# Performance work log

Hardware: AMD Instinct MI355X
Metric: run time of the kernel (lower is better)

## Reference

```python
import jax, jax.numpy as jnp
import numpy as np

T = 4096
MOL = 2048
DESC = 6
NSOL = 5
H = 2048
D_BLOCK = MOL + DESC            # 2054
FUSE = D_BLOCK * (1 + NSOL)     # 12324
D_IN = FUSE + 1                 # 12325
BOUNDARY_RF = 0.5
CLAMP_LO, CLAMP_HI = 1e-4, 1.0 - 1e-4


def setup_inputs() -> dict:
    key = jax.random.key(0)
    ks = jax.random.split(key, 32)
    s = 0.02  # weight init scale for numerical stability
    d = {
        "mol_vec": jax.random.normal(ks[0], (MOL,), jnp.float32),
        "solvent_seq": jax.random.uniform(ks[1], (T, NSOL), jnp.float32),
        "desc_seq": jax.random.normal(ks[2], (T, DESC), jnp.float32),
        "rf_true": jax.random.uniform(ks[3], (T,), jnp.float32),
        "solvent_vecs": jax.random.normal(ks[4], (NSOL, MOL), jnp.float32),
    }
    wshapes = [
        ("Wf0", (H, D_IN)), ("Wf1", (H, H)), ("Wf2", (H, H)), ("Wof", (1, H)),
        ("Wb0", (H, D_IN)), ("Wb1", (H, H)), ("Wb2", (H, H)), ("Wob", (1, H)),
    ]
    for i, (name, shp) in enumerate(wshapes):
        d[name] = jax.random.normal(ks[5 + i], shp, jnp.float32) * s
    for name, shp in [("bf0", (H,)), ("bf1", (H,)), ("bf2", (H,)), ("bof", (1,)),
                      ("bb0", (H,)), ("bb1", (H,)), ("bb2", (H,)), ("bob", (1,))]:
        d[name] = jnp.zeros(shp, jnp.float32)
    return d


def _step_features(mol_vec, solvent_seq, desc_seq, solvent_vecs):
    # mol_vec [MOL]; solvent_seq [T,NSOL]; desc_seq [T,DESC]; solvent_vecs [NSOL,MOL]
    mol_cat = jnp.concatenate(
        [jnp.broadcast_to(mol_vec, (T, MOL)), desc_seq], axis=-1)  # [T, D_BLOCK]
    scaled = solvent_seq[:, :, None] * solvent_vecs[None, :, :]      # [T,NSOL,MOL]
    sol_block = jnp.concatenate(
        [scaled, jnp.broadcast_to(desc_seq[:, None, :], (T, NSOL, DESC))], axis=-1)
    sol_flat = sol_block.reshape(T, NSOL * D_BLOCK)
    return jnp.concatenate([mol_cat, sol_flat], axis=-1)             # [T, FUSE]


def _trunk(x, W0, b0, W1, b1, W2, b2):
    # 3 Linear+GELU blocks (dropout is identity in eval)
    h = jax.nn.gelu(x @ W0.T + b0, approximate=False)
    h = jax.nn.gelu(h @ W1.T + b1, approximate=False)
    h = jax.nn.gelu(h @ W2.T + b2, approximate=False)
    return h


def reference(mol_vec, solvent_seq, desc_seq, rf_true, solvent_vecs,
              Wf0, bf0, Wf1, bf1, Wf2, bf2, Wof, bof,
              Wb0, bb0, Wb1, bb1, Wb2, bb2, Wob, bob):
    x = _step_features(mol_vec, solvent_seq, desc_seq, solvent_vecs)  # [T, FUSE]
    rf = jax.lax.stop_gradient(rf_true)  # teacher signal is detached
    b = jnp.asarray([BOUNDARY_RF], dtype=x.dtype)
    prev = jnp.concatenate([b, rf[:-1]])  # fwd branch sees rf_true[t-1]
    nxt = jnp.concatenate([rf[1:], b])    # bwd branch sees rf_true[t+1]

    inp_f = jnp.concatenate([x, prev[:, None]], axis=-1)  # [T, D_IN]
    inp_b = jnp.concatenate([x, nxt[:, None]], axis=-1)

    hf = _trunk(inp_f, Wf0, bf0, Wf1, bf1, Wf2, bf2)
    hb = _trunk(inp_b, Wb0, bb0, Wb1, bb1, Wb2, bb2)
    rf_fwd = (hf @ Wof.T + bof).squeeze(-1)  # [T]
    rf_bwd = (hb @ Wob.T + bob).squeeze(-1)
    rf_fwd = jnp.clip(rf_fwd, CLAMP_LO, CLAMP_HI)
    rf_bwd = jnp.clip(rf_bwd, CLAMP_LO, CLAMP_HI)
    return rf_fwd, rf_bwd
```

## Files before the change

kernel.cpp:

```cpp
#include <hip/hip_runtime.h>
#include <hip/hip_fp16.h>
#include <math.h>

#define T_DIM 4096
#define MOL_N 2048
#define DESC_N 6
#define NSOL_N 5
#define H_DIM 2048
#define DBLK 2054
#define D_IN_N 12325
#define GK 2048

typedef _Float16 f16x8 __attribute__((ext_vector_type(8)));
typedef float f32x4 __attribute__((ext_vector_type(4)));

__device__ __forceinline__ float gelu_f(float x) {
    float v = x * (1.5957691f + 0.0713548f * x * x);
    float e = __expf(-v);
    return x / (1.0f + e);
}

__global__ __launch_bounds__(256) void fold3_kernel(
    const float* __restrict__ W0f, const float* __restrict__ W0b,
    const float* __restrict__ b0f, const float* __restrict__ b0b,
    const float* __restrict__ mol, const float* __restrict__ sv,
    float* __restrict__ fold_f, float* __restrict__ fold_b)
{
    __shared__ float red[4];
    const int r = blockIdx.x;
    const int s = blockIdx.y;
    const int z = r >> 11, h = r & 2047;
    const int tid = threadIdx.x;
    const float* __restrict__ W0 = z ? W0b : W0f;
    const float* __restrict__ b0 = z ? b0b : b0f;
    float* __restrict__ fold = z ? fold_b : fold_f;
    const float* __restrict__ row = W0 + (size_t)h * D_IN_N + (size_t)s * DBLK;
    const float* __restrict__ xp = (s == 0) ? mol : (sv + (size_t)(s - 1) * MOL_N);

    float acc = 0.f;
    #pragma unroll
    for (int k = 0; k < 8; ++k) {
        const int c = tid + k * 256;
        acc += row[c] * xp[c];
    }
    #pragma unroll
    for (int off = 32; off >= 1; off >>= 1)
        acc += __shfl_xor(acc, off, 64);
    const int lane = tid & 63, wave = tid >> 6;
    if (lane == 0) red[wave] = acc;
    __syncthreads();
    if (tid == 0) {
        float v = red[0] + red[1] + red[2] + red[3];
        if (s == 0) fold[h] = v + b0[h];
        else fold[(size_t)s * H_DIM + h] = v;
    }
    if (s == 0 && tid >= 64 && tid < 70) {
        const int j = tid - 64;
        const float* __restrict__ rw = W0 + (size_t)h * D_IN_N;
        float w = rw[MOL_N + j];
        #pragma unroll
        for (int ss = 1; ss <= 5; ++ss) w += rw[(size_t)DBLK * ss + MOL_N + j];
        fold[(size_t)(6 + j) * H_DIM + h] = w;
    }
    if (s == 0 && tid == 70) {
        const float* __restrict__ rw = W0 + (size_t)h * D_IN_N;
        fold[(size_t)12 * H_DIM + h] = rw[D_IN_N - 1];
    }
}

__global__ __launch_bounds__(256) void conv_kernel(
    const float* __restrict__ W1f, const float* __restrict__ W2f,
    const float* __restrict__ W1b, const float* __restrict__ W2b,
    _Float16* __restrict__ Wc)
{
    const int b = blockIdx.x;
    const int z = b >> 10;
    const float* __restrict__ src = (z == 0) ? W1f : (z == 1) ? W2f : (z == 2) ? W1b : W2b;
    _Float16* __restrict__ dst = Wc + (size_t)z * H_DIM * H_DIM;
    const int base4 = (b & 1023) * 1024;
    struct h4 { _Float16 a, b, c, d; };
    #pragma unroll
    for (int k = 0; k < 4; ++k) {
        const int i4 = base4 + k * 256 + threadIdx.x;
        float4 v = ((const float4*)src)[i4];
        h4 o;
        o.a = (_Float16)v.x; o.b = (_Float16)v.y; o.c = (_Float16)v.z; o.d = (_Float16)v.w;
        ((h4*)dst)[i4] = o;
    }
}

__global__ __launch_bounds__(256) void h0_kernel(
    const float* __restrict__ fold_f, const float* __restrict__ fold_b,
    const float* __restrict__ desc, const float* __restrict__ sol,
    const float* __restrict__ rf,
    _Float16* __restrict__ h0f, _Float16* __restrict__ h0b)
{
    const int z = blockIdx.z;
    const float* __restrict__ fold = z ? fold_b : fold_f;
    _Float16* __restrict__ h0 = z ? h0b : h0f;
    const int hb = blockIdx.x * 1024 + threadIdx.x * 4;
    const int tbase = blockIdx.y * 64;

    float c0a[4], wpa[4], ua[NSOL_N][4], wda[DESC_N][4];
    {
        float4 v = *(const float4*)&fold[hb];
        c0a[0] = v.x; c0a[1] = v.y; c0a[2] = v.z; c0a[3] = v.w;
        v = *(const float4*)&fold[(size_t)12 * H_DIM + hb];
        wpa[0] = v.x; wpa[1] = v.y; wpa[2] = v.z; wpa[3] = v.w;
        #pragma unroll
        for (int s = 0; s < NSOL_N; ++s) {
            v = *(const float4*)&fold[(size_t)(1 + s) * H_DIM + hb];
            ua[s][0] = v.x; ua[s][1] = v.y; ua[s][2] = v.z; ua[s][3] = v.w;
        }
        #pragma unroll
        for (int j = 0; j < DESC_N; ++j) {
            v = *(const float4*)&fold[(size_t)(6 + j) * H_DIM + hb];
            wda[j][0] = v.x; wda[j][1] = v.y; wda[j][2] = v.z; wda[j][3] = v.w;
        }
    }

    struct h4s { _Float16 a, b, c, d; };
    for (int i = 0; i < 64; ++i) {
        const int t = tbase + i;
        float pv;
        if (z == 0) pv = (t == 0) ? 0.5f : rf[t - 1];
        else        pv = (t == T_DIM - 1) ? 0.5f : rf[t + 1];
        float sl[NSOL_N], dc[DESC_N];
        #pragma unroll
        for (int s = 0; s < NSOL_N; ++s) sl[s] = sol[t * NSOL_N + s];
        #pragma unroll
        for (int j = 0; j < DESC_N; ++j) dc[j] = desc[t * DESC_N + j];
        float o[4];
        #pragma unroll
        for (int e = 0; e < 4; ++e) {
            float pre = c0a[e] + wpa[e] * pv;
            #pragma unroll
            for (int s = 0; s < NSOL_N; ++s) pre += ua[s][e] * sl[s];
            #pragma unroll
            for (int j = 0; j < DESC_N; ++j) pre += wda[j][e] * dc[j];
            o[e] = gelu_f(pre);
        }
        h4s ov;
        ov.a = (_Float16)o[0]; ov.b = (_Float16)o[1];
        ov.c = (_Float16)o[2]; ov.d = (_Float16)o[3];
        *(h4s*)&h0[(size_t)t * H_DIM + hb] = ov;
    }
}

__device__ __forceinline__ void gemm_core256(
    const _Float16* __restrict__ A, const _Float16* __restrict__ W,
    const int m0, const int n0, char* sc, f32x4 (&acc)[8][4])
{
    const int tid = threadIdx.x;
    const int wave = tid >> 6;
    const int lane = tid & 63;
    const int t15 = lane & 15;
    const int quad = lane >> 4;
    const int wr = wave >> 2;
    const int wc = wave & 3;
    const int poff = (quad ^ ((t15 >> 1) & 3)) * 16;
    const int aoff0 = (wr * 128 + t15) * 64 + poff;
    const int boff0 = 16384 + (wc * 64 + t15) * 64 + poff;

    const _Float16* gsrc[4];
    #pragma unroll
    for (int ld = 0; ld < 4; ++ld) {
        const int j = (ld & 1) * 512 + tid;
        const int r = j >> 2;
        const int c = (j & 3) ^ ((r >> 1) & 3);
        gsrc[ld] = ((ld < 2) ? (A + (size_t)(m0 + r) * GK)
                             : (W + (size_t)(n0 + r) * GK)) + c * 8;
    }

    #pragma unroll
    for (int mi = 0; mi < 8; ++mi)
        #pragma unroll
        for (int ni = 0; ni < 4; ++ni)
            acc[mi][ni] = (f32x4){0.f, 0.f, 0.f, 0.f};

#define STAGE_T(kt, b) do { \
    char* _db = sc + (b) * 32768; \
    const int _ko = (kt) * 32; \
    __builtin_amdgcn_global_load_lds((const __attribute__((address_space(1))) void*)(gsrc[0] + _ko), (__attribute__((address_space(3))) void*)(_db + wave * 1024), 16, 0, 0); \
    __builtin_amdgcn_global_load_lds((const __attribute__((address_space(1))) void*)(gsrc[1] + _ko), (__attribute__((address_space(3))) void*)(_db + 8192 + wave * 1024), 16, 0, 0); \
    __builtin_amdgcn_global_load_lds((const __attribute__((address_space(1))) void*)(gsrc[2] + _ko), (__attribute__((address_space(3))) void*)(_db + 16384 + wave * 1024), 16, 0, 0); \
    __builtin_amdgcn_global_load_lds((const __attribute__((address_space(1))) void*)(gsrc[3] + _ko), (__attribute__((address_space(3))) void*)(_db + 24576 + wave * 1024), 16, 0, 0); \
} while (0)

#define COMPUTE_T(b) do { \
    const char* _db = sc + (b) * 32768; \
    f16x8 aF[8], bF[4]; \
    _Pragma("unroll") \
    for (int mi = 0; mi < 8; ++mi) aF[mi] = *(const f16x8*)(_db + aoff0 + mi * 1024); \
    _Pragma("unroll") \
    for (int ni = 0; ni < 4; ++ni) bF[ni] = *(const f16x8*)(_db + boff0 + ni * 1024); \
    __builtin_amdgcn_s_setprio(1); \
    _Pragma("unroll") \
    for (int mi = 0; mi < 8; ++mi) { \
        _Pragma("unroll") \
        for (int ni = 0; ni < 4; ++ni) \
            acc[mi][ni] = __builtin_amdgcn_mfma_f32_16x16x32_f16(aF[mi], bF[ni], acc[mi][ni], 0, 0, 0); \
    } \
    __builtin_amdgcn_s_setprio(0); \
    asm volatile("s_waitcnt lgkmcnt(0)" ::: "memory"); \
} while (0)

    STAGE_T(0, 0); STAGE_T(1, 1); STAGE_T(2, 2);

    #pragma unroll 1
    for (int k4 = 0; k4 < 60; k4 += 4) {
        asm volatile("s_waitcnt vmcnt(8)" ::: "memory");
        __builtin_amdgcn_s_barrier();
        STAGE_T(k4 + 3, 3); COMPUTE_T(0);
        asm volatile("s_waitcnt vmcnt(8)" ::: "memory");
        __builtin_amdgcn_s_barrier();
        STAGE_T(k4 + 4, 0); COMPUTE_T(1);
        asm volatile("s_waitcnt vmcnt(8)" ::: "memory");
        __builtin_amdgcn_s_barrier();
        STAGE_T(k4 + 5, 1); COMPUTE_T(2);
        asm volatile("s_waitcnt vmcnt(8)" ::: "memory");
        __builtin_amdgcn_s_barrier();
        STAGE_T(k4 + 6, 2); COMPUTE_T(3);
    }
    asm volatile("s_waitcnt vmcnt(8)" ::: "memory");
    __builtin_amdgcn_s_barrier();
    STAGE_T(63, 3); COMPUTE_T(0);
    asm volatile("s_waitcnt vmcnt(8)" ::: "memory");
    __builtin_amdgcn_s_barrier();
    COMPUTE_T(1);
    asm volatile("s_waitcnt vmcnt(4)" ::: "memory");
    __builtin_amdgcn_s_barrier();
    COMPUTE_T(2);
    asm volatile("s_waitcnt vmcnt(0)" ::: "memory");
    __builtin_amdgcn_s_barrier();
    COMPUTE_T(3);

#undef STAGE_T
#undef COMPUTE_T
}

__device__ __forceinline__ void tile_map(int bid, int& z, int& m0, int& n0, int& n_tile)
{
    const int xcd = bid & 7;
    const int slot = bid >> 3;
    z = xcd & 1;
    const int q = xcd >> 1;
    m0 = (slot & 15) * 256;
    n_tile = q * 2 + (slot >> 4);
    n0 = n_tile * 256;
}

__global__ __launch_bounds__(512, 2) void gemm1_kernel(
    const _Float16* __restrict__ Af, const _Float16* __restrict__ Ab,
    const _Float16* __restrict__ Wfp, const _Float16* __restrict__ Wbp,
    const float* __restrict__ bfp, const float* __restrict__ bbp,
    _Float16* __restrict__ Cf, _Float16* __restrict__ Cb)
{
    __shared__ _Float16 smem[65536];
    char* sc = (char*)smem;
    int z, m0, n0, n_tile;
    tile_map(blockIdx.x, z, m0, n0, n_tile);

    const _Float16* __restrict__ A = z ? Ab : Af;
    const _Float16* __restrict__ W = z ? Wbp : Wfp;
    const float* __restrict__ bias = z ? bbp : bfp;
    _Float16* __restrict__ C = z ? Cb : Cf;

    f32x4 acc[8][4];
    gemm_core256(A, W, m0, n0, sc, acc);

    const int tid = threadIdx.x;
    const int wave = tid >> 6, lane = tid & 63;
    const int colC = lane & 15, quad = lane >> 4;
    const int wr = wave >> 2, wc = wave & 3;
    #pragma unroll
    for (int ni = 0; ni < 4; ++ni) {
        const int n = n0 + wc * 64 + ni * 16 + colC;
        const float bv = bias[n];
        #pragma unroll
        for (int mi = 0; mi < 8; ++mi) {
            const int mb = m0 + wr * 128 + mi * 16 + quad * 4;
            #pragma unroll
            for (int r = 0; r < 4; ++r)
                C[(size_t)(mb + r) * H_DIM + n] = (_Float16)gelu_f(acc[mi][ni][r] + bv);
        }
    }
}

__global__ __launch_bounds__(512, 2) void gemm_out_kernel(
    const _Float16* __restrict__ Af, const _Float16* __restrict__ Ab,
    const _Float16* __restrict__ Wfp, const _Float16* __restrict__ Wbp,
    const float* __restrict__ bfp, const float* __restrict__ bbp,
    const float* __restrict__ Wof, const float* __restrict__ Wob,
    float* __restrict__ partial)
{
    __shared__ _Float16 smem[65536];
    char* sc = (char*)smem;
    int z, m0, n0, n_tile;
    tile_map(blockIdx.x, z, m0, n0, n_tile);

    const _Float16* __restrict__ A = z ? Ab : Af;
    const _Float16* __restrict__ W = z ? Wbp : Wfp;
    const float* __restrict__ bias = z ? bbp : bfp;
    const float* __restrict__ Wo = z ? Wob : Wof;

    f32x4 acc[8][4];
    gemm_core256(A, W, m0, n0, sc, acc);

    const int tid = threadIdx.x;
    const int wave = tid >> 6, lane = tid & 63;
    const int colC = lane & 15, quad = lane >> 4;
    const int wr = wave >> 2, wc = wave & 3;

    float bv[4], wo[4];
    #pragma unroll
    for (int ni = 0; ni < 4; ++ni) {
        const int n = n0 + wc * 64 + ni * 16 + colC;
        bv[ni] = bias[n];
        wo[ni] = Wo[n];
    }

    __syncthreads();
    float* red = (float*)sc;
    #pragma unroll
    for (int mi = 0; mi < 8; ++mi) {
        #pragma unroll
        for (int r = 0; r < 4; ++r) {
            float s = 0.f;
            #pragma unroll
            for (int ni = 0; ni < 4; ++ni)
                s += gelu_f(acc[mi][ni][r] + bv[ni]) * wo[ni];
            s += __shfl_xor(s, 1, 64);
            s += __shfl_xor(s, 2, 64);
            s += __shfl_xor(s, 4, 64);
            s += __shfl_xor(s, 8, 64);
            if (colC == 0)
                red[wc * 256 + wr * 128 + mi * 16 + quad * 4 + r] = s;
        }
    }
    __syncthreads();
    if (tid < 256) {
        float v = red[tid] + red[256 + tid] + red[512 + tid] + red[768 + tid];
        partial[((size_t)z * 8 + n_tile) * T_DIM + m0 + tid] = v;
    }
}

__global__ __launch_bounds__(256) void finalize_kernel(
    const float* __restrict__ partial,
    const float* __restrict__ bof, const float* __restrict__ bob,
    float* __restrict__ out)
{
    const int idx = blockIdx.x * 256 + threadIdx.x;
    const int z = idx >> 12;
    const int row = idx & 4095;
    float v = z ? bob[0] : bof[0];
    #pragma unroll
    for (int nt = 0; nt < 8; ++nt)
        v += partial[((size_t)z * 8 + nt) * T_DIM + row];
    v = fminf(fmaxf(v, 1e-4f), 1.0f - 1e-4f);
    out[idx] = v;
}

extern "C" void kernel_launch(void* const* d_in, const int* in_sizes, int n_in,
                              void* d_out, int out_size, void* d_ws, size_t ws_size,
                              hipStream_t stream)
{
    (void)in_sizes; (void)n_in; (void)out_size; (void)ws_size;
    const float* mol = (const float*)d_in[0];
    const float* sol = (const float*)d_in[1];
    const float* desc = (const float*)d_in[2];
    const float* rf  = (const float*)d_in[3];
    const float* sv  = (const float*)d_in[4];
    const float* Wf0 = (const float*)d_in[5];
    const float* Wf1 = (const float*)d_in[6];
    const float* Wf2 = (const float*)d_in[7];
    const float* Wof = (const float*)d_in[8];
    const float* Wb0 = (const float*)d_in[9];
    const float* Wb1 = (const float*)d_in[10];
    const float* Wb2 = (const float*)d_in[11];
    const float* Wob = (const float*)d_in[12];
    const float* bf0 = (const float*)d_in[13];
    const float* bf1 = (const float*)d_in[14];
    const float* bf2 = (const float*)d_in[15];
    const float* bof = (const float*)d_in[16];
    const float* bb0 = (const float*)d_in[17];
    const float* bb1 = (const float*)d_in[18];
    const float* bb2 = (const float*)d_in[19];
    const float* bob = (const float*)d_in[20];
    float* out = (float*)d_out;

    char* ws = (char*)d_ws;
    float* fold_f = (float*)(ws + 0);
    float* fold_b = (float*)(ws + 131072);
    _Float16* Wc = (_Float16*)(ws + 262144);
    const size_t WSZ = (size_t)H_DIM * H_DIM;
    _Float16* W1f_c = Wc;
    _Float16* W2f_c = Wc + WSZ;
    _Float16* W1b_c = Wc + 2 * WSZ;
    _Float16* W2b_c = Wc + 3 * WSZ;
    const size_t HSZ = (size_t)T_DIM * H_DIM;
    _Float16* h0f = (_Float16*)(ws + 33816576);
    _Float16* h0b = h0f + HSZ;
    _Float16* h1f = (_Float16*)(ws + 33816576 + 2 * 16777216);
    _Float16* h1b = h1f + HSZ;
    float* partial = (float*)(ws + 33816576);

    fold3_kernel<<<dim3(4096, 6), 256, 0, stream>>>(Wf0, Wb0, bf0, bb0, mol, sv, fold_f, fold_b);
    conv_kernel<<<dim3(4096), 256, 0, stream>>>(Wf1, Wf2, Wb1, Wb2, Wc);
    h0_kernel<<<dim3(2, 64, 2), 256, 0, stream>>>(fold_f, fold_b, desc, sol, rf, h0f, h0b);
    gemm1_kernel<<<dim3(256), 512, 0, stream>>>(h0f, h0b, W1f_c, W1b_c, bf1, bb1, h1f, h1b);
    gemm_out_kernel<<<dim3(256), 512, 0, stream>>>(h1f, h1b, W2f_c, W2b_c, bf2, bb2, Wof, Wob, partial);
    finalize_kernel<<<dim3(32), 256, 0, stream>>>(partial, bof, bob, out);
}
```

Baseline: 487.3 us.

## Merge fold and weight-convert kernels, deepen load waits, remap GEMM tiles per XCD

Merges the W0 fold kernel and the fp16 weight conversion kernel into one launch with a flat grid, and batches their global loads before use. It also relaxes the vmcnt waits in the GEMM pipeline from 8 to 16 outstanding loads so more prefetches stay in flight. Finally it changes the tile-to-XCD mapping so each XCD covers 4 M-tiles across all N-tiles instead of 16 M-tiles across 2 N-tiles, which changes L2 reuse of A versus W. The wait-count change must still match the number of loads per stage, or it risks reading LDS data before it has arrived.

```diff
diff --git a/kernel.cpp b/kernel.cpp
--- a/kernel.cpp
+++ b/kernel.cpp
@@ -20,29 +20,58 @@
     return x / (1.0f + e);
 }
 
-__global__ __launch_bounds__(256) void fold3_kernel(
+__global__ __launch_bounds__(256) void prep2_kernel(
+    const float* __restrict__ W1f, const float* __restrict__ W2f,
+    const float* __restrict__ W1b, const float* __restrict__ W2b,
+    _Float16* __restrict__ Wc,
     const float* __restrict__ W0f, const float* __restrict__ W0b,
     const float* __restrict__ b0f, const float* __restrict__ b0b,
     const float* __restrict__ mol, const float* __restrict__ sv,
     float* __restrict__ fold_f, float* __restrict__ fold_b)
 {
     __shared__ float red[4];
-    const int r = blockIdx.x;
-    const int s = blockIdx.y;
+    const int bid = blockIdx.x;
+    const int tid = threadIdx.x;
+
+    if (bid < 4096) {
+        const int z = bid >> 10;
+        const float* __restrict__ src = (z == 0) ? W1f : (z == 1) ? W2f : (z == 2) ? W1b : W2b;
+        _Float16* __restrict__ dst = Wc + (size_t)z * H_DIM * H_DIM;
+        const int base4 = (bid & 1023) * 1024;
+        float4 v[4];
+        #pragma unroll
+        for (int k = 0; k < 4; ++k)
+            v[k] = ((const float4*)src)[base4 + k * 256 + tid];
+        struct h4 { _Float16 a, b, c, d; };
+        #pragma unroll
+        for (int k = 0; k < 4; ++k) {
+            h4 o;
+            o.a = (_Float16)v[k].x; o.b = (_Float16)v[k].y;
+            o.c = (_Float16)v[k].z; o.d = (_Float16)v[k].w;
+            ((h4*)dst)[base4 + k * 256 + tid] = o;
+        }
+        return;
+    }
+
+    const int fb = bid - 4096;
+    const int r = fb & 4095;
+    const int s = fb >> 12;
     const int z = r >> 11, h = r & 2047;
-    const int tid = threadIdx.x;
     const float* __restrict__ W0 = z ? W0b : W0f;
     const float* __restrict__ b0 = z ? b0b : b0f;
     float* __restrict__ fold = z ? fold_b : fold_f;
     const float* __restrict__ row = W0 + (size_t)h * D_IN_N + (size_t)s * DBLK;
     const float* __restrict__ xp = (s == 0) ? mol : (sv + (size_t)(s - 1) * MOL_N);
 
+    float w[8], x[8];
+    #pragma unroll
+    for (int k = 0; k < 8; ++k) w[k] = row[tid + k * 256];
+    #pragma unroll
+    for (int k = 0; k < 8; ++k) x[k] = xp[tid + k * 256];
     float acc = 0.f;
     #pragma unroll
-    for (int k = 0; k < 8; ++k) {
-        const int c = tid + k * 256;
-        acc += row[c] * xp[c];
-    }
+    for (int k = 0; k < 8; ++k) acc += w[k] * x[k];
+
     #pragma unroll
     for (int off = 32; off >= 1; off >>= 1)
         acc += __shfl_xor(acc, off, 64);
@@ -57,35 +86,14 @@
     if (s == 0 && tid >= 64 && tid < 70) {
         const int j = tid - 64;
         const float* __restrict__ rw = W0 + (size_t)h * D_IN_N;
-        float w = rw[MOL_N + j];
-        #pragma unroll
-        for (int ss = 1; ss <= 5; ++ss) w += rw[(size_t)DBLK * ss + MOL_N + j];
-        fold[(size_t)(6 + j) * H_DIM + h] = w;
+        float ww = rw[MOL_N + j];
+        #pragma unroll
+        for (int ss = 1; ss <= 5; ++ss) ww += rw[(size_t)DBLK * ss + MOL_N + j];
+        fold[(size_t)(6 + j) * H_DIM + h] = ww;
     }
     if (s == 0 && tid == 70) {
         const float* __restrict__ rw = W0 + (size_t)h * D_IN_N;
         fold[(size_t)12 * H_DIM + h] = rw[D_IN_N - 1];
-    }
-}
-
-__global__ __launch_bounds__(256) void conv_kernel(
-    const float* __restrict__ W1f, const float* __restrict__ W2f,
-    const float* __restrict__ W1b, const float* __restrict__ W2b,
-    _Float16* __restrict__ Wc)
-{
-    const int b = blockIdx.x;
-    const int z = b >> 10;
-    const float* __restrict__ src = (z == 0) ? W1f : (z == 1) ? W2f : (z == 2) ? W1b : W2b;
-    _Float16* __restrict__ dst = Wc + (size_t)z * H_DIM * H_DIM;
-    const int base4 = (b & 1023) * 1024;
-    struct h4 { _Float16 a, b, c, d; };
-    #pragma unroll
-    for (int k = 0; k < 4; ++k) {
-        const int i4 = base4 + k * 256 + threadIdx.x;
-        float4 v = ((const float4*)src)[i4];
-        h4 o;
-        o.a = (_Float16)v.x; o.b = (_Float16)v.y; o.c = (_Float16)v.z; o.d = (_Float16)v.w;
-        ((h4*)dst)[i4] = o;
     }
 }
 
@@ -209,26 +217,26 @@
 
     #pragma unroll 1
     for (int k4 = 0; k4 < 60; k4 += 4) {
-        asm volatile("s_waitcnt vmcnt(8)" ::: "memory");
+        asm volatile("s_waitcnt vmcnt(16)" ::: "memory");
         __builtin_amdgcn_s_barrier();
         STAGE_T(k4 + 3, 3); COMPUTE_T(0);
-        asm volatile("s_waitcnt vmcnt(8)" ::: "memory");
+        asm volatile("s_waitcnt vmcnt(16)" ::: "memory");
         __builtin_amdgcn_s_barrier();
         STAGE_T(k4 + 4, 0); COMPUTE_T(1);
-        asm volatile("s_waitcnt vmcnt(8)" ::: "memory");
+        asm volatile("s_waitcnt vmcnt(16)" ::: "memory");
         __builtin_amdgcn_s_barrier();
         STAGE_T(k4 + 5, 1); COMPUTE_T(2);
-        asm volatile("s_waitcnt vmcnt(8)" ::: "memory");
+        asm volatile("s_waitcnt vmcnt(16)" ::: "memory");
         __builtin_amdgcn_s_barrier();
         STAGE_T(k4 + 6, 2); COMPUTE_T(3);
     }
-    asm volatile("s_waitcnt vmcnt(8)" ::: "memory");
+    asm volatile("s_waitcnt vmcnt(16)" ::: "memory");
     __builtin_amdgcn_s_barrier();
     STAGE_T(63, 3); COMPUTE_T(0);
-    asm volatile("s_waitcnt vmcnt(8)" ::: "memory");
+    asm volatile("s_waitcnt vmcnt(16)" ::: "memory");
     __builtin_amdgcn_s_barrier();
     COMPUTE_T(1);
-    asm volatile("s_waitcnt vmcnt(4)" ::: "memory");
+    asm volatile("s_waitcnt vmcnt(8)" ::: "memory");
     __builtin_amdgcn_s_barrier();
     COMPUTE_T(2);
     asm volatile("s_waitcnt vmcnt(0)" ::: "memory");
@@ -245,8 +253,8 @@
     const int slot = bid >> 3;
     z = xcd & 1;
     const int q = xcd >> 1;
-    m0 = (slot & 15) * 256;
-    n_tile = q * 2 + (slot >> 4);
+    m0 = (q * 4 + (slot & 3)) * 256;
+    n_tile = slot >> 2;
     n0 = n_tile * 256;
 }
 
@@ -405,8 +413,8 @@
     _Float16* h1b = h1f + HSZ;
     float* partial = (float*)(ws + 33816576);
 
-    fold3_kernel<<<dim3(4096, 6), 256, 0, stream>>>(Wf0, Wb0, bf0, bb0, mol, sv, fold_f, fold_b);
-    conv_kernel<<<dim3(4096), 256, 0, stream>>>(Wf1, Wf2, Wb1, Wb2, Wc);
+    prep2_kernel<<<dim3(28672), 256, 0, stream>>>(
+        Wf1, Wf2, Wb1, Wb2, Wc, Wf0, Wb0, bf0, bb0, mol, sv, fold_f, fold_b);
     h0_kernel<<<dim3(2, 64, 2), 256, 0, stream>>>(fold_f, fold_b, desc, sol, rf, h0f, h0b);
     gemm1_kernel<<<dim3(256), 512, 0, stream>>>(h0f, h0b, W1f_c, W1b_c, bf1, bb1, h1f, h1b);
     gemm_out_kernel<<<dim3(256), 512, 0, stream>>>(h1f, h1b, W2f_c, W2b_c, bf2, bb2, Wof, Wob, partial);
```

Measured after the change: 483.7 us. About the same (-0.7%).
